# Kernel tuning notes

Hardware: AMD Instinct MI355X
Metric: run time of the kernel (lower is better)

The kernel has to match this reference:

```python
import jax, jax.numpy as jnp
import numpy as np

N = 1024
IN_DIM = 64
H = 8
D = 8
E_REAL = 16384
GAMMA = 0.1


def setup_inputs() -> dict:
    key = jax.random.key(0)
    ks = jax.random.split(key, 12)
    inp = {
        "h": jax.random.normal(ks[0], (N, IN_DIM), dtype=jnp.float32),
        "e": jax.random.normal(ks[1], (E_REAL, IN_DIM), dtype=jnp.float32),
        "WQ": jax.random.normal(ks[2], (IN_DIM, H * D), dtype=jnp.float32) * 0.1,
        "WK": jax.random.normal(ks[3], (IN_DIM, H * D), dtype=jnp.float32) * 0.1,
        "WE": jax.random.normal(ks[4], (IN_DIM, H * D), dtype=jnp.float32) * 0.1,
        "WQ2": jax.random.normal(ks[5], (IN_DIM, H * D), dtype=jnp.float32) * 0.1,
        "WK2": jax.random.normal(ks[6], (IN_DIM, H * D), dtype=jnp.float32) * 0.1,
        "WE2": jax.random.normal(ks[7], (IN_DIM, H * D), dtype=jnp.float32) * 0.1,
        "WV": jax.random.normal(ks[8], (IN_DIM, H * D), dtype=jnp.float32) * 0.1,
        "real_src": jax.random.randint(ks[9], (E_REAL,), 0, N, dtype=jnp.int32),
        "real_dst": jax.random.randint(ks[10], (E_REAL,), 0, N, dtype=jnp.int32),
    }
    return inp


def reference(h, e, WQ, WK, WE, WQ2, WK2, WE2, WV, real_src, real_dst):
    scale = float(np.sqrt(D))
    # Dense edge-feature adjacency: adj[src, dst] = e  (zeros elsewhere)
    adj = jnp.zeros((N, N, IN_DIM), dtype=h.dtype).at[real_src, real_dst].set(e)
    # Edge projections over the dense adjacency (no bias): [N, N, H, D]
    Eh = (adj @ WE).reshape(N, N, H, D)
    E2h = (adj @ WE2).reshape(N, N, H, D)
    # Node projections: [N, H, D]
    Qh = (h @ WQ).reshape(N, H, D)
    Kh = (h @ WK).reshape(N, H, D)
    Q2h = (h @ WQ2).reshape(N, H, D)
    K2h = (h @ WK2).reshape(N, H, D)
    Vh = (h @ WV).reshape(N, H, D)
    # 3-way K*Q*E contraction over head dim: [N, N, H] (i = src, j = dst)
    weights_real = jnp.einsum('ihd,jhd,ijhd->ijh', Kh, Qh, Eh) / scale
    weights_fake = jnp.einsum('ihd,jhd,ijhd->ijh', K2h, Q2h, E2h) / scale
    weights_real_exp = jnp.exp(jnp.clip(weights_real, -5.0, 5.0)) / (GAMMA + 1.0)
    weights_fake_exp = GAMMA * jnp.exp(jnp.clip(weights_fake, -5.0, 5.0)) / (GAMMA + 1.0)
    # Blend: real-edge positions take the real attention value
    weights_final = weights_fake_exp.at[real_src, real_dst].set(
        weights_real_exp[real_src, real_dst])
    # Zero self-loops
    idx = jnp.arange(N)
    weights_final = weights_final.at[idx, idx].set(0.0)
    # Aggregate values at destination nodes: sum over src i -> [N, H, D]
    out = jnp.einsum('ijh,ihd->jhd', weights_final, Vh)
    # Normalizer: sum of attention weights per destination node [N, H, 1]
    z = jnp.sum(weights_final, axis=0).reshape(N, H, 1)
    return out / (z + 1e-6)
```

## Files before the change

### kernel.cpp

```cpp
#include <hip/hip_runtime.h>

#define NN     1024
#define INDIM  64
#define EREAL  16384
#define HD     64

constexpr float C_BASE    = 0.1f / 1.1f;
constexpr float INV_1P1   = 1.0f / 1.1f;
constexpr float INV_SCALE = 0.35355339059327373f;

__device__ __forceinline__ float bcast(float v, int lane) {
    return __uint_as_float(__builtin_amdgcn_readlane(__float_as_uint(v), lane));
}

__global__ __launch_bounds__(256)
void prep_kernel(const float* __restrict__ h,
                 const float* __restrict__ WQ,
                 const float* __restrict__ WK,
                 const float* __restrict__ WV,
                 const int*   __restrict__ src,
                 const int*   __restrict__ dst,
                 float* __restrict__ Qh,
                 float* __restrict__ Kh,
                 float* __restrict__ Vh,
                 float* __restrict__ Spart,
                 int*   __restrict__ winner)
{
    const int tid = threadIdx.x;
    const int bid = blockIdx.x;
    const int g = tid >> 6, c = tid & 63;
    __shared__ float lds_buf[4][64];

    if (bid < 256) {
        const int row = bid * 4 + g;
        lds_buf[g][c] = h[row * INDIM + c];
        __syncthreads();
        float q = 0.f, k = 0.f, v = 0.f;
#pragma unroll
        for (int r = 0; r < INDIM; ++r) {
            const float hv = lds_buf[g][r];
            q = fmaf(hv, WQ[r * HD + c], q);
            k = fmaf(hv, WK[r * HD + c], k);
            v = fmaf(hv, WV[r * HD + c], v);
        }
        Qh[row * HD + c] = q;
        Kh[row * HD + c] = k;
        Vh[row * HD + c] = v;
    } else if (bid < 320) {
        const int k = (bid - 256) * 256 + tid;
        atomicMax(&winner[src[k] * NN + dst[k]], k + 1);
    } else {
        const int p = bid - 320;
        float s = 0.f;
        const int j0 = p * 64 + g * 16;
        for (int j = j0; j < j0 + 16; ++j) s += h[j * INDIM + c];
        lds_buf[g][c] = s;
        __syncthreads();
        if (g == 0)
            Spart[p * INDIM + c] = lds_buf[0][c] + lds_buf[1][c] + lds_buf[2][c] + lds_buf[3][c];
    }
}

__global__ __launch_bounds__(256)
void edge_kernel(const float* __restrict__ e,
                 const float* __restrict__ WE,
                 const float* __restrict__ Qh,
                 const float* __restrict__ Kh,
                 const float* __restrict__ Vh,
                 const int*   __restrict__ src,
                 const int*   __restrict__ dst,
                 const int*   __restrict__ winner,
                 float* __restrict__ outacc,
                 float* __restrict__ zacc)
{
    const int gtid = blockIdx.x * 256 + threadIdx.x;
    const int wave = gtid >> 6;
    const int t    = threadIdx.x & 63;
    const int k0   = wave * 8;

    float ev[8];
#pragma unroll
    for (int i = 0; i < 8; ++i) ev[i] = e[(k0 + i) * INDIM + t];
    float acc[8] = {0.f, 0.f, 0.f, 0.f, 0.f, 0.f, 0.f, 0.f};
#pragma unroll
    for (int r = 0; r < INDIM; ++r) {
        const float w = WE[r * HD + t];
#pragma unroll
        for (int i = 0; i < 8; ++i)
            acc[i] = fmaf(bcast(ev[i], r), w, acc[i]);
    }
#pragma unroll
    for (int i = 0; i < 8; ++i) {
        const int k = k0 + i;
        const int s = src[k];
        const int d = dst[k];
        if (winner[s * NN + d] != k + 1 || s == d) continue;
        float term = Kh[s * HD + t] * Qh[d * HD + t] * acc[i];
        term += __shfl_xor(term, 1, 64);
        term += __shfl_xor(term, 2, 64);
        term += __shfl_xor(term, 4, 64);
        const float wr    = fminf(fmaxf(term * INV_SCALE, -5.f), 5.f);
        const float delta = __expf(wr) * INV_1P1 - C_BASE;
        atomicAdd(&outacc[d * HD + t], delta * Vh[s * HD + t]);
        if ((t & 7) == 0) atomicAdd(&zacc[d * 8 + (t >> 3)], delta);
    }
}

__global__ __launch_bounds__(256)
void finalize_kernel(const float* __restrict__ WV,
                     const float* __restrict__ Vh,
                     const float* __restrict__ Spart,
                     const float* __restrict__ outacc,
                     const float* __restrict__ zacc,
                     float* __restrict__ out)
{
    const int tid = threadIdx.x;
    __shared__ float sh_hsum[INDIM];
    __shared__ float sh_S[HD];
    if (tid < INDIM) {
        float hs = 0.f;
#pragma unroll
        for (int p = 0; p < 16; ++p) hs += Spart[p * INDIM + tid];
        sh_hsum[tid] = hs;
    }
    __syncthreads();
    if (tid < HD) {
        float s = 0.f;
#pragma unroll
        for (int r = 0; r < INDIM; ++r) s += sh_hsum[r] * WV[r * HD + tid];
        sh_S[tid] = s;
    }
    __syncthreads();
    const int idx = blockIdx.x * 256 + tid;
    const int j = idx >> 6, t = idx & 63;
    const float z = C_BASE * 1023.f + zacc[j * 8 + (t >> 3)] + 1e-6f;
    out[idx] = fmaf(C_BASE, sh_S[t] - Vh[idx], outacc[idx]) / z;
}

extern "C" void kernel_launch(void* const* d_in, const int* in_sizes, int n_in,
                              void* d_out, int out_size, void* d_ws, size_t ws_size,
                              hipStream_t stream) {
    const float* h  = (const float*)d_in[0];
    const float* e  = (const float*)d_in[1];
    const float* WQ = (const float*)d_in[2];
    const float* WK = (const float*)d_in[3];
    const float* WE = (const float*)d_in[4];
    const float* WV = (const float*)d_in[8];
    const int* src  = (const int*)d_in[9];
    const int* dst  = (const int*)d_in[10];
    float* out = (float*)d_out;

    char* ws = (char*)d_ws;
    float* Qh     = (float*)(ws + (0    << 10));
    float* Kh     = (float*)(ws + (256  << 10));
    float* Vh     = (float*)(ws + (512  << 10));
    float* Spart  = (float*)(ws + (768  << 10));
    float* outacc = (float*)(ws + (1024 << 10));
    float* zacc   = (float*)(ws + (1280 << 10));
    int*   winner = (int*)  (ws + (1312 << 10));
    const size_t zbytes = (288 << 10) + (4u << 20);

    hipMemsetAsync(outacc, 0, zbytes, stream);
    hipLaunchKernelGGL(prep_kernel, dim3(336), dim3(256), 0, stream,
                       h, WQ, WK, WV, src, dst, Qh, Kh, Vh, Spart, winner);
    hipLaunchKernelGGL(edge_kernel, dim3(512), dim3(256), 0, stream,
                       e, WE, Qh, Kh, Vh, src, dst, winner, outacc, zacc);
    hipLaunchKernelGGL(finalize_kernel, dim3(256), dim3(256), 0, stream,
                       WV, Vh, Spart, outacc, zacc, out);
}
```

Before: 101.3 us.

## Fold buffer zeroing into prep kernel and resolve duplicate edges in edge kernel

Drops the separate memset: the prep kernel now zeroes the winner table and the output/normalizer accumulators with float4 stores in extra blocks. The atomicMax duplicate-edge resolution moves from the prep kernel into the edge kernel. When an edge displaces an earlier winner, the kernel recomputes that winner's edge projection and subtracts its contribution. This removes a memset launch and the separate scatter pass. The cost is extra atomics and occasional recomputation of a 64x64 projection for duplicate edges, plus correctness that relies on the additions and subtractions commuting.

```diff
diff --git a/kernel.cpp b/kernel.cpp
--- a/kernel.cpp
+++ b/kernel.cpp
@@ -18,18 +18,18 @@
                  const float* __restrict__ WQ,
                  const float* __restrict__ WK,
                  const float* __restrict__ WV,
-                 const int*   __restrict__ src,
-                 const int*   __restrict__ dst,
                  float* __restrict__ Qh,
                  float* __restrict__ Kh,
                  float* __restrict__ Vh,
                  float* __restrict__ Spart,
+                 float* __restrict__ outacc,
                  int*   __restrict__ winner)
 {
     const int tid = threadIdx.x;
     const int bid = blockIdx.x;
     const int g = tid >> 6, c = tid & 63;
     __shared__ float lds_buf[4][64];
+    const float4 zero4 = make_float4(0.f, 0.f, 0.f, 0.f);
 
     if (bid < 256) {
         const int row = bid * 4 + g;
@@ -46,11 +46,16 @@
         Qh[row * HD + c] = q;
         Kh[row * HD + c] = k;
         Vh[row * HD + c] = v;
-    } else if (bid < 320) {
-        const int k = (bid - 256) * 256 + tid;
-        atomicMax(&winner[src[k] * NN + dst[k]], k + 1);
+    } else if (bid < 512) {
+        const int idx = (bid - 256) * 256 + tid;
+        float4* w4 = (float4*)winner;
+#pragma unroll
+        for (int i = 0; i < 4; ++i) w4[idx + i * 65536] = zero4;
+    } else if (bid < 584) {
+        const int idx = (bid - 512) * 256 + tid;
+        ((float4*)outacc)[idx] = zero4;
     } else {
-        const int p = bid - 320;
+        const int p = bid - 584;
         float s = 0.f;
         const int j0 = p * 64 + g * 16;
         for (int j = j0; j < j0 + 16; ++j) s += h[j * INDIM + c];
@@ -69,7 +74,7 @@
                  const float* __restrict__ Vh,
                  const int*   __restrict__ src,
                  const int*   __restrict__ dst,
-                 const int*   __restrict__ winner,
+                 int*   __restrict__ winner,
                  float* __restrict__ outacc,
                  float* __restrict__ zacc)
 {
@@ -94,15 +99,38 @@
         const int k = k0 + i;
         const int s = src[k];
         const int d = dst[k];
-        if (winner[s * NN + d] != k + 1 || s == d) continue;
-        float term = Kh[s * HD + t] * Qh[d * HD + t] * acc[i];
+        if (s == d) continue;
+        const float kq = Kh[s * HD + t] * Qh[d * HD + t];
+        float term = kq * acc[i];
         term += __shfl_xor(term, 1, 64);
         term += __shfl_xor(term, 2, 64);
         term += __shfl_xor(term, 4, 64);
         const float wr    = fminf(fmaxf(term * INV_SCALE, -5.f), 5.f);
         const float delta = __expf(wr) * INV_1P1 - C_BASE;
+
+        int ret = 0;
+        if (t == 0) ret = atomicMax(&winner[s * NN + d], k + 1);
+        ret = __shfl(ret, 0, 64);
+
+        if (ret > k + 1) continue;
         atomicAdd(&outacc[d * HD + t], delta * Vh[s * HD + t]);
         if ((t & 7) == 0) atomicAdd(&zacc[d * 8 + (t >> 3)], delta);
+        if (ret >= 1) {
+            const int j = ret - 1;
+            const float evj = e[j * INDIM + t];
+            float accj = 0.f;
+#pragma unroll
+            for (int r = 0; r < INDIM; ++r)
+                accj = fmaf(bcast(evj, r), WE[r * HD + t], accj);
+            float termj = kq * accj;
+            termj += __shfl_xor(termj, 1, 64);
+            termj += __shfl_xor(termj, 2, 64);
+            termj += __shfl_xor(termj, 4, 64);
+            const float wrj    = fminf(fmaxf(termj * INV_SCALE, -5.f), 5.f);
+            const float deltaj = __expf(wrj) * INV_1P1 - C_BASE;
+            atomicAdd(&outacc[d * HD + t], -deltaj * Vh[s * HD + t]);
+            if ((t & 7) == 0) atomicAdd(&zacc[d * 8 + (t >> 3)], -deltaj);
+        }
     }
 }
 
@@ -158,11 +186,9 @@
     float* outacc = (float*)(ws + (1024 << 10));
     float* zacc   = (float*)(ws + (1280 << 10));
     int*   winner = (int*)  (ws + (1312 << 10));
-    const size_t zbytes = (288 << 10) + (4u << 20);
 
-    hipMemsetAsync(outacc, 0, zbytes, stream);
-    hipLaunchKernelGGL(prep_kernel, dim3(336), dim3(256), 0, stream,
-                       h, WQ, WK, WV, src, dst, Qh, Kh, Vh, Spart, winner);
+    hipLaunchKernelGGL(prep_kernel, dim3(600), dim3(256), 0, stream,
+                       h, WQ, WK, WV, Qh, Kh, Vh, Spart, outacc, winner);
     hipLaunchKernelGGL(edge_kernel, dim3(512), dim3(256), 0, stream,
                        e, WE, Qh, Kh, Vh, src, dst, winner, outacc, zacc);
     hipLaunchKernelGGL(finalize_kernel, dim3(256), dim3(256), 0, stream,
```

Measured after the change: 103.7 us. 1.02x slower.
